# Kernel tuning notes

Measured on AMD Instinct MI355X. Metric: run time of the kernel, lower is better.

The kernel has to match this reference:

```python
import jax, jax.numpy as jnp
import numpy as np

B, N, S, D, H = 8, 64, 128, 512, 8
DK = D // H


def setup_inputs() -> dict:
    key = jax.random.key(0)
    ks = jax.random.split(key, 8)
    x = jax.random.normal(ks[0], (B, N, S, D), dtype=jnp.float32)
    mask = jax.random.randint(ks[1], (B, N, S), 0, 2).astype(jnp.int32)
    mask = mask.at[..., 0].set(1)  # guarantee at least one valid token per sentence
    w = 1.0 / np.sqrt(D).astype(np.float32)
    Wq = jax.random.normal(ks[2], (D, D), dtype=jnp.float32) * w
    Wk = jax.random.normal(ks[3], (D, D), dtype=jnp.float32) * w
    Wv = jax.random.normal(ks[4], (D, D), dtype=jnp.float32) * w
    Wo = jax.random.normal(ks[5], (D, D), dtype=jnp.float32) * w
    bq = jnp.zeros((D,), jnp.float32)
    bk = jnp.zeros((D,), jnp.float32)
    bv = jnp.zeros((D,), jnp.float32)
    bo = jnp.zeros((D,), jnp.float32)
    sent_q = jax.random.normal(ks[6], (H, DK), dtype=jnp.float32)
    return {"x": x, "mask": mask, "Wq": Wq, "bq": bq, "Wk": Wk, "bk": bk,
            "Wv": Wv, "bv": bv, "sent_q": sent_q, "Wo": Wo, "bo": bo}


def reference(x, mask, Wq, bq, Wk, bk, Wv, bv, sent_q, Wo, bo):
    b, n, s, d = x.shape
    h, dk = sent_q.shape
    inv_sqrt_dk = 1.0 / np.sqrt(dk).astype(np.float32)
    # QKV projections, split heads: (B, N, S, H, dk)
    Q = (x @ Wq + bq).reshape(b, n, s, h, dk)
    K = (x @ Wk + bk).reshape(b, n, s, h, dk)
    V = (x @ Wv + bv).reshape(b, n, s, h, dk)
    # sentence-query attention over tokens within each sentence: (B, H, N, S)
    sent_scores = jnp.einsum('hd,bnshd->bhns', sent_q, K) * inv_sqrt_dk
    sent_scores = jnp.where(mask[:, None, :, :] == 0, jnp.float32(-1e9), sent_scores)
    sent_attn = jax.nn.softmax(sent_scores, axis=-1)
    # pooled per-sentence representation: (B, H, N, dk)
    sent_repr = jnp.einsum('bhns,bnshd->bhnd', sent_attn, V)
    # degenerate token softmax over a single key (== 1), kept faithfully
    token_scores = jnp.einsum('bnshd,bhnd->bhns', Q, sent_repr) * inv_sqrt_dk
    token_attn = jax.nn.softmax(token_scores[..., None], axis=-1)[..., 0]  # (B,H,N,S), all ones
    # broadcast pooled repr to every token, scale by (unit) attn: (B, H, N, S, dk)
    out = token_attn[..., None] * sent_repr[:, :, :, None, :]
    out = jnp.transpose(out, (0, 2, 3, 1, 4)).reshape(b, n, s, d)
    return out @ Wo + bo
```

## Files before the change

### kernel.cpp

```cpp
#include <hip/hip_runtime.h>
#include <math.h>

#define BB 8
#define NN 64
#define SS 128
#define DD 512
#define HH 8
#define DKK 64

__global__ void precompute_wk(const float* __restrict__ Wk,
                              const float* __restrict__ sq,
                              float* __restrict__ wk_t) {
    const int d = threadIdx.x;
    const int h = blockIdx.x;
    const float4* wrow = (const float4*)(Wk + (size_t)d * DD + h * DKK);
    const float4* sqv  = (const float4*)(sq + h * DKK);
    float acc = 0.f;
#pragma unroll
    for (int k = 0; k < DKK / 4; ++k) {
        float4 w = wrow[k], q = sqv[k];
        acc += w.x * q.x + w.y * q.y + w.z * q.z + w.w * q.w;
    }
    wk_t[h * DD + d] = acc;
}

__global__ __launch_bounds__(512, 4)
void sent_attn_kernel(const float* __restrict__ x,
                      const int* __restrict__ mask,
                      const float* __restrict__ wk_t,
                      const float* __restrict__ Wv,
                      const float* __restrict__ bv,
                      const float* __restrict__ Wo,
                      const float* __restrict__ bo,
                      float* __restrict__ out) {
    __shared__ float sc[HH][SS];
    __shared__ float xbar[HH][DD];
    __shared__ float zsh[DD];

    const int bid  = blockIdx.x;
    const int t    = threadIdx.x;
    const int wave = t >> 6;
    const int lane = t & 63;
    const float* xt = x + (size_t)bid * SS * DD;

    const int d0 = lane * 8;
    float4 wkA[HH], wkB[HH];
#pragma unroll
    for (int h = 0; h < HH; ++h) {
        wkA[h] = *(const float4*)(wk_t + h * DD + d0);
        wkB[h] = *(const float4*)(wk_t + h * DD + d0 + 4);
    }

    for (int s = wave; s < SS; s += 8) {
        const float* xr = xt + s * DD + d0;
        float4 xa = *(const float4*)xr;
        float4 xb = *(const float4*)(xr + 4);
        float p[HH];
#pragma unroll
        for (int h = 0; h < HH; ++h) {
            p[h] = xa.x * wkA[h].x + xa.y * wkA[h].y + xa.z * wkA[h].z + xa.w * wkA[h].w
                 + xb.x * wkB[h].x + xb.y * wkB[h].y + xb.z * wkB[h].z + xb.w * wkB[h].w;
        }
#pragma unroll
        for (int off = 32; off > 0; off >>= 1) {
#pragma unroll
            for (int h = 0; h < HH; ++h)
                p[h] += __shfl_down(p[h], off, 64);
        }
        if (lane == 0) {
            const int m = mask[bid * SS + s];
#pragma unroll
            for (int h = 0; h < HH; ++h)
                sc[h][s] = (m == 0) ? -1e9f : p[h] * 0.125f;
        }
    }
    __syncthreads();

    {
        const int h = wave;
        float v0 = sc[h][lane], v1 = sc[h][lane + 64];
        float m = fmaxf(v0, v1);
#pragma unroll
        for (int off = 32; off > 0; off >>= 1)
            m = fmaxf(m, __shfl_xor(m, off, 64));
        float e0 = __expf(v0 - m);
        float e1 = __expf(v1 - m);
        float ssum = e0 + e1;
#pragma unroll
        for (int off = 32; off > 0; off >>= 1)
            ssum += __shfl_xor(ssum, off, 64);
        float inv = 1.0f / ssum;
        sc[h][lane]      = e0 * inv;
        sc[h][lane + 64] = e1 * inv;
    }
    __syncthreads();

    {
        float acc[HH];
#pragma unroll
        for (int h = 0; h < HH; ++h) acc[h] = 0.f;
#pragma unroll 4
        for (int s = 0; s < SS; ++s) {
            float xv = xt[(size_t)s * DD + t];
#pragma unroll
            for (int h = 0; h < HH; ++h)
                acc[h] += sc[h][s] * xv;
        }
#pragma unroll
        for (int h = 0; h < HH; ++h) xbar[h][t] = acc[h];
    }
    __syncthreads();

    {
        const int h = t >> 6;
        const float* wvp = Wv + t;
        const float* xb  = &xbar[h][0];
        float a0 = 0.f, a1 = 0.f, a2 = 0.f, a3 = 0.f;
#pragma unroll 4
        for (int d = 0; d < DD; d += 4) {
            a0 += xb[d + 0] * wvp[(size_t)(d + 0) * DD];
            a1 += xb[d + 1] * wvp[(size_t)(d + 1) * DD];
            a2 += xb[d + 2] * wvp[(size_t)(d + 2) * DD];
            a3 += xb[d + 3] * wvp[(size_t)(d + 3) * DD];
        }
        zsh[t] = bv[t] + ((a0 + a1) + (a2 + a3));
    }
    __syncthreads();

    {
        const float* wop = Wo + t;
        float a0 = 0.f, a1 = 0.f, a2 = 0.f, a3 = 0.f;
#pragma unroll 4
        for (int d = 0; d < DD; d += 4) {
            a0 += zsh[d + 0] * wop[(size_t)(d + 0) * DD];
            a1 += zsh[d + 1] * wop[(size_t)(d + 1) * DD];
            a2 += zsh[d + 2] * wop[(size_t)(d + 2) * DD];
            a3 += zsh[d + 3] * wop[(size_t)(d + 3) * DD];
        }
        const float y = bo[t] + ((a0 + a1) + (a2 + a3));
        float* op = out + (size_t)bid * SS * DD + t;
#pragma unroll 4
        for (int s = 0; s < SS; ++s)
            op[(size_t)s * DD] = y;
    }
}

extern "C" void kernel_launch(void* const* d_in, const int* in_sizes, int n_in,
                              void* d_out, int out_size, void* d_ws, size_t ws_size,
                              hipStream_t stream) {
    const float* x    = (const float*)d_in[0];
    const int*   mask = (const int*)  d_in[1];
    const float* Wk   = (const float*)d_in[4];
    const float* Wv   = (const float*)d_in[6];
    const float* bv   = (const float*)d_in[7];
    const float* sq   = (const float*)d_in[8];
    const float* Wo   = (const float*)d_in[9];
    const float* bo   = (const float*)d_in[10];
    float* out  = (float*)d_out;
    float* wk_t = (float*)d_ws;

    precompute_wk<<<HH, DD, 0, stream>>>(Wk, sq, wk_t);
    sent_attn_kernel<<<BB * NN, DD, 0, stream>>>(x, mask, wk_t, Wv, bv, Wo, bo, out);
}
```

Measured before the change: 118.6 us.

## Split sentence attention into pipelined pooling, batched GEMMs, and broadcast kernels

The fused per-sentence kernel is replaced by four kernels. The first streams x through LDS in double-buffered tiles using global_load_lds and computes the masked softmax weights online without a max subtraction. Per-head pooled x is written into scratch space inside the output buffer. Two tiled 64x64 GEMMs then apply Wv and Wo across all 512 sentences at once, so each block no longer rereads the full weight matrices, and a final kernel broadcasts the result to every token. The risks are extra launches, round trips through the output buffer, and possible overflow in the exp without max subtraction.

```diff
diff --git a/kernel.cpp b/kernel.cpp
--- a/kernel.cpp
+++ b/kernel.cpp
@@ -7,6 +7,16 @@
 #define DD 512
 #define HH 8
 #define DKK 64
+#define TS 16
+#define NT (SS / TS)
+
+#define SENT_STRIDE (SS * DD)
+#define Y_OFF  0
+#define Z_OFF  DD
+#define XB_OFF (2 * DD)
+
+#define GLOBAL_AS(p) ((const __attribute__((address_space(1))) void*)(p))
+#define LDS_AS(p)    ((__attribute__((address_space(3))) void*)(p))
 
 __global__ void precompute_wk(const float* __restrict__ Wk,
                               const float* __restrict__ sq,
@@ -25,23 +35,21 @@
 }
 
 __global__ __launch_bounds__(512, 4)
-void sent_attn_kernel(const float* __restrict__ x,
-                      const int* __restrict__ mask,
-                      const float* __restrict__ wk_t,
-                      const float* __restrict__ Wv,
-                      const float* __restrict__ bv,
-                      const float* __restrict__ Wo,
-                      const float* __restrict__ bo,
-                      float* __restrict__ out) {
-    __shared__ float sc[HH][SS];
-    __shared__ float xbar[HH][DD];
-    __shared__ float zsh[DD];
+void k1_xbar(const float* __restrict__ x, const int* __restrict__ mask,
+             const float* __restrict__ wk_t, float* __restrict__ outp)
+{
+    __shared__ float xl[2][TS][DD];
+    __shared__ float wl[HH][SS];
+    __shared__ float wsum_sh[HH];
+    __shared__ int   ml[SS];
 
     const int bid  = blockIdx.x;
     const int t    = threadIdx.x;
     const int wave = t >> 6;
     const int lane = t & 63;
-    const float* xt = x + (size_t)bid * SS * DD;
+    const float* xs = x + (size_t)bid * SENT_STRIDE;
+
+    if (t < SS) ml[t] = mask[bid * SS + t];
 
     const int d0 = lane * 8;
     float4 wkA[HH], wkB[HH];
@@ -51,98 +59,164 @@
         wkB[h] = *(const float4*)(wk_t + h * DD + d0 + 4);
     }
 
-    for (int s = wave; s < SS; s += 8) {
-        const float* xr = xt + s * DD + d0;
-        float4 xa = *(const float4*)xr;
-        float4 xb = *(const float4*)(xr + 4);
-        float p[HH];
-#pragma unroll
-        for (int h = 0; h < HH; ++h) {
-            p[h] = xa.x * wkA[h].x + xa.y * wkA[h].y + xa.z * wkA[h].z + xa.w * wkA[h].w
-                 + xb.x * wkB[h].x + xb.y * wkB[h].y + xb.z * wkB[h].z + xb.w * wkB[h].w;
+    float acc[HH];
+#pragma unroll
+    for (int h = 0; h < HH; ++h) acc[h] = 0.f;
+
+#define STAGE(buf, tile)                                                        \
+    do {                                                                        \
+        const float* g_ = xs + (tile) * (TS * DD) + wave * 1024 + lane * 4;     \
+        float* l_ = &xl[(buf)][0][0] + wave * 1024;                             \
+        __builtin_amdgcn_global_load_lds(GLOBAL_AS(g_ +   0), LDS_AS(l_ +   0), 16, 0, 0); \
+        __builtin_amdgcn_global_load_lds(GLOBAL_AS(g_ + 256), LDS_AS(l_ + 256), 16, 0, 0); \
+        __builtin_amdgcn_global_load_lds(GLOBAL_AS(g_ + 512), LDS_AS(l_ + 512), 16, 0, 0); \
+        __builtin_amdgcn_global_load_lds(GLOBAL_AS(g_ + 768), LDS_AS(l_ + 768), 16, 0, 0); \
+    } while (0)
+
+    STAGE(0, 0);
+
+    for (int tile = 0; tile < NT; ++tile) {
+        const int cur = tile & 1;
+        __syncthreads();
+        if (tile + 1 < NT) STAGE(cur ^ 1, tile + 1);
+
+#pragma unroll
+        for (int j = 0; j < 2; ++j) {
+            const int sl = wave * 2 + j;
+            const int sg = tile * TS + sl;
+            const float* xr = &xl[cur][sl][d0];
+            float4 xa = *(const float4*)xr;
+            float4 xb = *(const float4*)(xr + 4);
+            float p[HH];
+#pragma unroll
+            for (int h = 0; h < HH; ++h)
+                p[h] = xa.x * wkA[h].x + xa.y * wkA[h].y + xa.z * wkA[h].z + xa.w * wkA[h].w
+                     + xb.x * wkB[h].x + xb.y * wkB[h].y + xb.z * wkB[h].z + xb.w * wkB[h].w;
+#pragma unroll
+            for (int off = 1; off <= 4; off <<= 1)
+#pragma unroll
+                for (int h = 0; h < HH; ++h)
+                    p[h] += __shfl_xor(p[h], off, 64);
+            const int hsel = lane & 7;
+            float v = p[0];
+#pragma unroll
+            for (int h = 1; h < HH; ++h) v = (hsel == h) ? p[h] : v;
+#pragma unroll
+            for (int off = 8; off <= 32; off <<= 1)
+                v += __shfl_xor(v, off, 64);
+            if (lane < HH) {
+                const float e = (ml[sg] == 0) ? 0.f : __expf(v * 0.125f);
+                wl[lane][sg] = e;
+            }
         }
-#pragma unroll
-        for (int off = 32; off > 0; off >>= 1) {
-#pragma unroll
-            for (int h = 0; h < HH; ++h)
-                p[h] += __shfl_down(p[h], off, 64);
+        asm volatile("s_waitcnt lgkmcnt(0)" ::: "memory");
+        __builtin_amdgcn_s_barrier();
+
+#pragma unroll
+        for (int half = 0; half < 2; ++half) {
+            float xv[8];
+#pragma unroll
+            for (int s = 0; s < 8; ++s) xv[s] = xl[cur][half * 8 + s][t];
+#pragma unroll
+            for (int h = 0; h < HH; ++h) {
+                const float* wp = &wl[h][tile * TS + half * 8];
+                float4 w0 = *(const float4*)(wp);
+                float4 w1 = *(const float4*)(wp + 4);
+                acc[h] += w0.x * xv[0] + w0.y * xv[1] + w0.z * xv[2] + w0.w * xv[3]
+                        + w1.x * xv[4] + w1.y * xv[5] + w1.z * xv[6] + w1.w * xv[7];
+            }
         }
-        if (lane == 0) {
-            const int m = mask[bid * SS + s];
-#pragma unroll
-            for (int h = 0; h < HH; ++h)
-                sc[h][s] = (m == 0) ? -1e9f : p[h] * 0.125f;
+    }
+
+    {
+        float v = wl[wave][lane] + wl[wave][lane + 64];
+#pragma unroll
+        for (int off = 32; off > 0; off >>= 1)
+            v += __shfl_xor(v, off, 64);
+        if (lane == 0) wsum_sh[wave] = v;
+    }
+    __syncthreads();
+
+    float* xb = outp + (size_t)bid * SENT_STRIDE + XB_OFF;
+#pragma unroll
+    for (int h = 0; h < HH; ++h)
+        xb[h * DD + t] = acc[h] * (1.0f / wsum_sh[h]);
+#undef STAGE
+}
+
+__global__ __launch_bounds__(256)
+void gemm64(const float* __restrict__ A, const int acolstride,
+            const float* __restrict__ B, const float* __restrict__ bias,
+            float* __restrict__ C)
+{
+    __shared__ float As[64][17];
+    __shared__ float Bs[16][64];
+
+    const int bid = blockIdx.x;
+    const int nb  = bid & 7, mb = bid >> 3;
+    const int tid = threadIdx.x;
+    const int tr  = tid >> 4, tc = tid & 15;
+    const int ar  = tid >> 2, aq = tid & 3;
+    const int br  = tid >> 4, bc = tid & 15;
+
+    const float* Ab = A + (size_t)(mb * 64) * SENT_STRIDE + nb * acolstride;
+    const float* Bb = B + nb * 64;
+
+    float ac[4][4];
+#pragma unroll
+    for (int i = 0; i < 4; ++i)
+#pragma unroll
+        for (int j = 0; j < 4; ++j) ac[i][j] = 0.f;
+
+    for (int k0 = 0; k0 < DD; k0 += 16) {
+        float4 av  = *(const float4*)(Ab + (size_t)ar * SENT_STRIDE + k0 + aq * 4);
+        float4 bv4 = *(const float4*)(Bb + (size_t)(k0 + br) * DD + bc * 4);
+        As[ar][aq * 4 + 0] = av.x;
+        As[ar][aq * 4 + 1] = av.y;
+        As[ar][aq * 4 + 2] = av.z;
+        As[ar][aq * 4 + 3] = av.w;
+        *(float4*)&Bs[br][bc * 4] = bv4;
+        __syncthreads();
+#pragma unroll
+        for (int kk = 0; kk < 16; ++kk) {
+            const float a0 = As[tr * 4 + 0][kk];
+            const float a1 = As[tr * 4 + 1][kk];
+            const float a2 = As[tr * 4 + 2][kk];
+            const float a3 = As[tr * 4 + 3][kk];
+            const float4 b4 = *(const float4*)&Bs[kk][tc * 4];
+            ac[0][0] += a0 * b4.x; ac[0][1] += a0 * b4.y; ac[0][2] += a0 * b4.z; ac[0][3] += a0 * b4.w;
+            ac[1][0] += a1 * b4.x; ac[1][1] += a1 * b4.y; ac[1][2] += a1 * b4.z; ac[1][3] += a1 * b4.w;
+            ac[2][0] += a2 * b4.x; ac[2][1] += a2 * b4.y; ac[2][2] += a2 * b4.z; ac[2][3] += a2 * b4.w;
+            ac[3][0] += a3 * b4.x; ac[3][1] += a3 * b4.y; ac[3][2] += a3 * b4.z; ac[3][3] += a3 * b4.w;
         }
-    }
-    __syncthreads();
-
-    {
-        const int h = wave;
-        float v0 = sc[h][lane], v1 = sc[h][lane + 64];
-        float m = fmaxf(v0, v1);
-#pragma unroll
-        for (int off = 32; off > 0; off >>= 1)
-            m = fmaxf(m, __shfl_xor(m, off, 64));
-        float e0 = __expf(v0 - m);
-        float e1 = __expf(v1 - m);
-        float ssum = e0 + e1;
-#pragma unroll
-        for (int off = 32; off > 0; off >>= 1)
-            ssum += __shfl_xor(ssum, off, 64);
-        float inv = 1.0f / ssum;
-        sc[h][lane]      = e0 * inv;
-        sc[h][lane + 64] = e1 * inv;
-    }
-    __syncthreads();
-
-    {
-        float acc[HH];
-#pragma unroll
-        for (int h = 0; h < HH; ++h) acc[h] = 0.f;
-#pragma unroll 4
-        for (int s = 0; s < SS; ++s) {
-            float xv = xt[(size_t)s * DD + t];
-#pragma unroll
-            for (int h = 0; h < HH; ++h)
-                acc[h] += sc[h][s] * xv;
-        }
-#pragma unroll
-        for (int h = 0; h < HH; ++h) xbar[h][t] = acc[h];
-    }
-    __syncthreads();
-
-    {
-        const int h = t >> 6;
-        const float* wvp = Wv + t;
-        const float* xb  = &xbar[h][0];
-        float a0 = 0.f, a1 = 0.f, a2 = 0.f, a3 = 0.f;
-#pragma unroll 4
-        for (int d = 0; d < DD; d += 4) {
-            a0 += xb[d + 0] * wvp[(size_t)(d + 0) * DD];
-            a1 += xb[d + 1] * wvp[(size_t)(d + 1) * DD];
-            a2 += xb[d + 2] * wvp[(size_t)(d + 2) * DD];
-            a3 += xb[d + 3] * wvp[(size_t)(d + 3) * DD];
-        }
-        zsh[t] = bv[t] + ((a0 + a1) + (a2 + a3));
-    }
-    __syncthreads();
-
-    {
-        const float* wop = Wo + t;
-        float a0 = 0.f, a1 = 0.f, a2 = 0.f, a3 = 0.f;
-#pragma unroll 4
-        for (int d = 0; d < DD; d += 4) {
-            a0 += zsh[d + 0] * wop[(size_t)(d + 0) * DD];
-            a1 += zsh[d + 1] * wop[(size_t)(d + 1) * DD];
-            a2 += zsh[d + 2] * wop[(size_t)(d + 2) * DD];
-            a3 += zsh[d + 3] * wop[(size_t)(d + 3) * DD];
-        }
-        const float y = bo[t] + ((a0 + a1) + (a2 + a3));
-        float* op = out + (size_t)bid * SS * DD + t;
-#pragma unroll 4
-        for (int s = 0; s < SS; ++s)
-            op[(size_t)s * DD] = y;
-    }
+        __syncthreads();
+    }
+
+    const float4 bb = *(const float4*)(bias + nb * 64 + tc * 4);
+#pragma unroll
+    for (int i = 0; i < 4; ++i) {
+        float4 o;
+        o.x = ac[i][0] + bb.x;
+        o.y = ac[i][1] + bb.y;
+        o.z = ac[i][2] + bb.z;
+        o.w = ac[i][3] + bb.w;
+        *(float4*)(C + (size_t)(mb * 64 + tr * 4 + i) * SENT_STRIDE + nb * 64 + tc * 4) = o;
+    }
+}
+
+__global__ __launch_bounds__(256)
+void k4_broadcast(float* __restrict__ outp)
+{
+    const int sent = blockIdx.x >> 2, q = blockIdx.x & 3;
+    float* base = outp + (size_t)sent * SENT_STRIDE;
+    const int t = threadIdx.x;
+    const int c = t & 127;
+    const float4 y = *(const float4*)(base + c * 4);
+    const int r0 = q * 32 + (t >> 7);
+    float* w0 = base + (size_t)r0 * DD + c * 4;
+#pragma unroll
+    for (int i = 0; i < 16; ++i)
+        *(float4*)(w0 + (size_t)(i * 2) * DD) = y;
 }
 
 extern "C" void kernel_launch(void* const* d_in, const int* in_sizes, int n_in,
@@ -160,5 +234,8 @@
     float* wk_t = (float*)d_ws;
 
     precompute_wk<<<HH, DD, 0, stream>>>(Wk, sq, wk_t);
-    sent_attn_kernel<<<BB * NN, DD, 0, stream>>>(x, mask, wk_t, Wv, bv, Wo, bo, out);
-}
+    k1_xbar<<<BB * NN, DD, 0, stream>>>(x, mask, wk_t, out);
+    gemm64<<<64, 256, 0, stream>>>(out + XB_OFF, DD, Wv, bv, out + Z_OFF);
+    gemm64<<<64, 256, 0, stream>>>(out + Z_OFF, 0, Wo, bo, out + Y_OFF);
+    k4_broadcast<<<BB * NN * 4, 256, 0, stream>>>(out);
+}
```

Result: slower. 171.3 us (+44.4%).
